# Performance work log

Measured on AMD Instinct MI355X. Metric: run time of the kernel, lower is better.

The kernel has to match this reference:

```python
import jax, jax.numpy as jnp
import numpy as np

V = 1_000_000      # vocab_length
E = 64             # embedding_dimension
H = 4              # mos_heads
B = 1024           # batch
S = V // 45        # num_neg_samples = 22222


def setup_inputs() -> dict:
    key = jax.random.key(0)
    k1, k2, k3, k4, k5, k6 = jax.random.split(key, 6)
    inputs = jax.random.normal(k1, (B, E), dtype=jnp.float32)
    # valid class ids are 1..V (id 0 is reserved by the sampler)
    label = jax.random.randint(k2, (B,), 1, V + 1, dtype=jnp.int32)
    sampled_ids = jax.random.randint(k3, (S,), 1, V + 1, dtype=jnp.int32)
    emb = jax.random.normal(k4, (V + 1, E), dtype=jnp.float32) * 0.05
    # GlorotNormal stddevs
    proj_mat = jax.random.normal(k5, (H * E, E), dtype=jnp.float32) * np.float32(np.sqrt(2.0 / (H * E + E)))
    mix_mat = jax.random.normal(k6, (H, E), dtype=jnp.float32) * np.float32(np.sqrt(2.0 / (H + E)))
    biases = jnp.zeros((V + 1,), dtype=jnp.float32)
    return {"inputs": inputs, "emb": emb, "proj_mat": proj_mat,
            "mix_mat": mix_mat, "biases": biases,
            "label": label, "sampled_ids": sampled_ids}


def reference(inputs, emb, proj_mat, mix_mat, biases, label, sampled_ids):
    # projections per mixture head: [B, H, E]
    mos_proj = jnp.tanh(inputs @ proj_mat.T).reshape(B, H, E)
    # mixture weights pi: [B, H]
    pi = jax.nn.softmax(inputs @ mix_mat.T, axis=-1)

    # sampled-softmax log-Q correction (unique unigram sampler, uniform probs):
    # expected_count = -expm1(S * log1p(-p)), p = 1/V
    p = jnp.float32(1.0 / V)
    log_q = jnp.log(-jnp.expm1(S * jnp.log1p(-p)))

    # true-class logit per head: [B, H]
    true_w = emb[label]                                   # [B, E] gather
    true_logit = (jnp.einsum('bhe,be->bh', mos_proj, true_w)
                  + biases[label][:, None] - log_q)
    # sampled logits per head: [B, H, S]
    samp_w = emb[sampled_ids]                             # [S, E] gather
    samp_logits = (jnp.einsum('bhe,se->bhs', mos_proj, samp_w)
                   + biases[sampled_ids][None, None, :] - log_q)

    logits = jnp.concatenate([true_logit[:, :, None], samp_logits], axis=-1)  # [B, H, 1+S]
    head_probs = jax.nn.softmax(logits, axis=-1)
    # mixture over heads: [B, 1+S]
    probs = jnp.einsum('bh,bhs->bs', pi, head_probs)
    # sampled labels are one-hot at position 0 -> loss = -mean(log p[:,0])
    loss = -jnp.mean(jnp.log(probs[:, 0]))
    return probs, loss
```

## Files before the change

### kernel.cpp

```cpp
#include <hip/hip_runtime.h>

#define ED 64
#define HD 4
#define BD 1024
#define SNEG 22222
#define NT2 1408
#define SPAD2 22528
#define SP1 (SNEG+1)
#define LOGQ -3.81776242f
#define LOG2E 1.44269504f

typedef short bf16x8 __attribute__((ext_vector_type(8)));
typedef float f32x4 __attribute__((ext_vector_type(4)));

static __device__ __forceinline__ short f2bf(float f) {
    union { float f; unsigned u; } v; v.f = f;
    return (short)((v.u + 0x7FFFu + ((v.u >> 16) & 1u)) >> 16);
}

static __device__ __forceinline__ float fast_tanh(float x) {
    float ax = __builtin_fabsf(x);
    float e  = __expf(-2.f * ax);
    float t  = (1.f - e) / (1.f + e);
    return __builtin_copysignf(t, x);
}

static __device__ __forceinline__ float fexp2(float x) {
#if __has_builtin(__builtin_amdgcn_exp2f)
    return __builtin_amdgcn_exp2f(x);
#else
    return __expf(x * 0.69314718f);
#endif
}

__global__ __launch_bounds__(256) void k_setup(
        const float* __restrict__ inputs, const float* __restrict__ emb,
        const float* __restrict__ proj,   const float* __restrict__ mix,
        const float* __restrict__ biases, const int* __restrict__ label,
        const int* __restrict__ sids,
        short* __restrict__ A, float* __restrict__ pi, float* __restrict__ tl,
        short* __restrict__ W, float* __restrict__ bias_s,
        float* __restrict__ denom) {
    const int blk = blockIdx.x, t = threadIdx.x;
    __shared__ float s_in[64];
    __shared__ float s_proj[256];
    __shared__ float s_mix[4];
    __shared__ float s_red[256];

    if (t < 16) denom[blk*16 + t] = 0.f;

    #pragma unroll 1
    for (int bi = 0; bi < 4; ++bi) {
        int b = blk*4 + bi;
        if (t < 64) s_in[t] = inputs[b*64 + t];
        __syncthreads();
        const float* pr = proj + t*64;
        float dot = 0.f;
        #pragma unroll
        for (int k = 0; k < 64; k += 4)
            dot += s_in[k]*pr[k] + s_in[k+1]*pr[k+1] + s_in[k+2]*pr[k+2] + s_in[k+3]*pr[k+3];
        float val = fast_tanh(dot);
        s_proj[t] = val;
        A[(b*4 + (t >> 6))*64 + (t & 63)] = f2bf(val * LOG2E);
        if (t < 4) {
            const float* mr = mix + t*64;
            float md = 0.f;
            for (int k = 0; k < 64; ++k) md += s_in[k]*mr[k];
            s_mix[t] = md;
        }
        int lab = label[b];
        s_red[t] = s_proj[t] * emb[(size_t)lab*64 + (t & 63)];
        __syncthreads();
        if (t < 4) {
            float m = fmaxf(fmaxf(s_mix[0], s_mix[1]), fmaxf(s_mix[2], s_mix[3]));
            float e0 = __expf(s_mix[0]-m), e1 = __expf(s_mix[1]-m);
            float e2 = __expf(s_mix[2]-m), e3 = __expf(s_mix[3]-m);
            pi[b*4 + t] = __expf(s_mix[t]-m) / (e0+e1+e2+e3);
            float sum = 0.f;
            for (int k = 0; k < 64; ++k) sum += s_red[t*64 + k];
            tl[b*4 + t] = (sum + biases[lab] - LOGQ) * LOG2E;
        }
        __syncthreads();
    }

    #pragma unroll 1
    for (int rep = 0; rep < 3; ++rep) {
        int task = rep*256 + t;
        if (task >= 704) break;
        int s = blk*88 + (task >> 3);
        int l8 = task & 7;
        if (s < SNEG) {
            int id = sids[s];
            const float* src = emb + (size_t)id*64 + l8*8;
            bf16x8 o;
            #pragma unroll
            for (int j = 0; j < 8; ++j) o[j] = f2bf(src[j]);
            *(bf16x8*)(W + s*64 + l8*8) = o;
            if (l8 == 0) bias_s[s] = (biases[id] - LOGQ) * LOG2E;
        } else {
            bf16x8 o;
            #pragma unroll
            for (int j = 0; j < 8; ++j) o[j] = 0;
            *(bf16x8*)(W + s*64 + l8*8) = o;
            if (l8 == 0) bias_s[s] = -1e30f;
        }
    }
}

#define LOADT(S, T) { \
    const bf16x8* bp_ = (const bf16x8*)(W + (size_t)((T)*16 + c)*64); \
    b0##S = bp_[g]; b1##S = bp_[4 + g]; bb##S = bias_s[(T)*16 + c]; }

#define DCOMP(S) { \
    _Pragma("unroll") \
    for (int t4 = 0; t4 < 4; ++t4) { \
        f32x4 z = {bb##S, bb##S, bb##S, bb##S}; \
        z = __builtin_amdgcn_mfma_f32_16x16x32_bf16(a0[t4], b0##S, z, 0, 0, 0); \
        z = __builtin_amdgcn_mfma_f32_16x16x32_bf16(a1[t4], b1##S, z, 0, 0, 0); \
        s[t4*4+0] += fexp2(z[0]); \
        s[t4*4+1] += fexp2(z[1]); \
        s[t4*4+2] += fexp2(z[2]); \
        s[t4*4+3] += fexp2(z[3]); } }

#define PCOMP(S, T) { \
    int scol_ = (T)*16 + c; bool ok_ = scol_ < SNEG; \
    _Pragma("unroll") \
    for (int t4 = 0; t4 < 4; ++t4) { \
        f32x4 z = {bb##S, bb##S, bb##S, bb##S}; \
        z = __builtin_amdgcn_mfma_f32_16x16x32_bf16(a0[t4], b0##S, z, 0, 0, 0); \
        z = __builtin_amdgcn_mfma_f32_16x16x32_bf16(a1[t4], b1##S, z, 0, 0, 0); \
        float p_ = cf[t4][0]*fexp2(z[0]); \
        p_ = fmaf(cf[t4][1], fexp2(z[1]), p_); \
        p_ = fmaf(cf[t4][2], fexp2(z[2]), p_); \
        p_ = fmaf(cf[t4][3], fexp2(z[3]), p_); \
        if (ok_) orow[t4][scol_] = p_; } }

#define DPIPE(TB) { \
    LOADT(A, (TB)+0) LOADT(B, (TB)+1) LOADT(C, (TB)+2) \
    DCOMP(A) LOADT(A, (TB)+3) \
    DCOMP(B) LOADT(B, (TB)+4) \
    DCOMP(C) LOADT(C, (TB)+5) \
    DCOMP(A) LOADT(A, (TB)+6) \
    DCOMP(B) LOADT(B, (TB)+7) \
    DCOMP(C) LOADT(C, (TB)+8) \
    DCOMP(A) LOADT(A, (TB)+9) \
    DCOMP(B) LOADT(B, (TB)+10) \
    DCOMP(C) \
    DCOMP(A) \
    DCOMP(B) }

#define PPIPE(TB) { \
    LOADT(A, (TB)+0) LOADT(B, (TB)+1) LOADT(C, (TB)+2) \
    PCOMP(A, (TB)+0)  LOADT(A, (TB)+3) \
    PCOMP(B, (TB)+1)  LOADT(B, (TB)+4) \
    PCOMP(C, (TB)+2)  LOADT(C, (TB)+5) \
    PCOMP(A, (TB)+3)  LOADT(A, (TB)+6) \
    PCOMP(B, (TB)+4)  LOADT(B, (TB)+7) \
    PCOMP(C, (TB)+5)  LOADT(C, (TB)+8) \
    PCOMP(A, (TB)+6)  LOADT(A, (TB)+9) \
    PCOMP(B, (TB)+7)  LOADT(B, (TB)+10) \
    PCOMP(C, (TB)+8) \
    PCOMP(A, (TB)+9) \
    PCOMP(B, (TB)+10) }

__global__ __launch_bounds__(256, 4) void k_denom(
        const short* __restrict__ A, const short* __restrict__ W,
        const float* __restrict__ bias_s, float* __restrict__ denom) {
    const int wave = threadIdx.x >> 6, lane = threadIdx.x & 63;
    const int g = lane >> 4, c = lane & 15;
    const int rbase = blockIdx.y * 64;
    bf16x8 a0[4], a1[4];
    #pragma unroll
    for (int t4 = 0; t4 < 4; ++t4) {
        const bf16x8* ap = (const bf16x8*)(A + (size_t)(rbase + t4*16 + c)*64);
        a0[t4] = ap[g]; a1[t4] = ap[4 + g];
    }
    float s[16];
    #pragma unroll
    for (int i = 0; i < 16; ++i) s[i] = 0.f;

    const int t0 = (blockIdx.x*4 + wave) * 44;
    bf16x8 b0A, b1A, b0B, b1B, b0C, b1C;
    float bbA, bbB, bbC;
    DPIPE(t0)
    DPIPE(t0 + 11)
    DPIPE(t0 + 22)
    DPIPE(t0 + 33)

    #pragma unroll
    for (int m = 1; m < 16; m <<= 1)
        #pragma unroll
        for (int i = 0; i < 16; ++i) s[i] += __shfl_xor(s[i], m);
    if (c == 0) {
        #pragma unroll
        for (int t4 = 0; t4 < 4; ++t4)
            #pragma unroll
            for (int r = 0; r < 4; ++r)
                atomicAdd(&denom[rbase + t4*16 + g*4 + r], s[t4*4+r]);
    }
}

__global__ __launch_bounds__(256, 4) void k_probs(
        const short* __restrict__ A, const short* __restrict__ W,
        const float* __restrict__ bias_s, const float* __restrict__ pi,
        const float* __restrict__ tl, const float* __restrict__ denom,
        float* __restrict__ out) {
    const int t = threadIdx.x;
    const int wave = t >> 6, lane = t & 63;
    const int g = lane >> 4, c = lane & 15;
    const int rbase = blockIdx.y * 64;
    __shared__ float s_cf[64];
    __shared__ float s_et[64];
    __shared__ float s_ls[4];

    if (t < 64) {
        int row = rbase + t;
        float et = fexp2(tl[row]);
        float d  = denom[row] + et;
        s_cf[t] = pi[row] / d;
        s_et[t] = et;
    }
    __syncthreads();
    if (blockIdx.x == 0 && t < 16) {
        float p0 = 0.f;
        #pragma unroll
        for (int h = 0; h < 4; ++h) p0 += s_cf[t*4 + h] * s_et[t*4 + h];
        out[(size_t)(rbase/4 + t) * SP1] = p0;
    }
    if (blockIdx.x == 0 && blockIdx.y == 0) {
        float lg = 0.f;
        for (int b = t; b < BD; b += 256) {
            float p0 = 0.f;
            #pragma unroll
            for (int h = 0; h < 4; ++h) {
                float et = fexp2(tl[b*4 + h]);
                p0 += pi[b*4 + h] / (denom[b*4 + h] + et) * et;
            }
            lg += logf(p0);
        }
        #pragma unroll
        for (int m = 1; m < 64; m <<= 1) lg += __shfl_xor(lg, m);
        if (lane == 0) s_ls[wave] = lg;
        __syncthreads();
        if (t == 0)
            out[(size_t)BD * SP1] = -(s_ls[0]+s_ls[1]+s_ls[2]+s_ls[3]) * (1.f/(float)BD);
    }

    bf16x8 a0[4], a1[4];
    float cf[4][4];
    float* orow[4];
    #pragma unroll
    for (int t4 = 0; t4 < 4; ++t4) {
        const bf16x8* ap = (const bf16x8*)(A + (size_t)(rbase + t4*16 + c)*64);
        a0[t4] = ap[g]; a1[t4] = ap[4 + g];
        #pragma unroll
        for (int r = 0; r < 4; ++r) cf[t4][r] = s_cf[t4*16 + g*4 + r];
        orow[t4] = out + (size_t)(rbase/4 + t4*4 + g) * SP1 + 1;
    }

    const int t0 = (blockIdx.x*4 + wave) * 44;
    bf16x8 b0A, b1A, b0B, b1B, b0C, b1C;
    float bbA, bbB, bbC;
    PPIPE(t0)
    PPIPE(t0 + 11)
    PPIPE(t0 + 22)
    PPIPE(t0 + 33)
}

extern "C" void kernel_launch(void* const* d_in, const int* in_sizes, int n_in,
                              void* d_out, int out_size, void* d_ws, size_t ws_size,
                              hipStream_t stream) {
    const float* inputs = (const float*)d_in[0];
    const float* emb    = (const float*)d_in[1];
    const float* proj   = (const float*)d_in[2];
    const float* mix    = (const float*)d_in[3];
    const float* biases = (const float*)d_in[4];
    const int*   label  = (const int*)d_in[5];
    const int*   sids   = (const int*)d_in[6];
    float* out = (float*)d_out;

    char* ws = (char*)d_ws;
    short* W      = (short*)(ws);
    short* A      = (short*)(ws + 2883584);
    float* bias_s = (float*)(ws + 3407872);
    float* denom  = (float*)(ws + 3497984);
    float* pi     = (float*)(ws + 3514368);
    float* tl     = (float*)(ws + 3530752);

    k_setup<<<256, 256, 0, stream>>>(
        inputs, emb, proj, mix, biases, label, sids, A, pi, tl, W, bias_s, denom);
    k_denom<<<dim3(8, 64), 256, 0, stream>>>(A, W, bias_s, denom);
    k_probs<<<dim3(8, 64), 256, 0, stream>>>(A, W, bias_s, pi, tl, denom, out);
}
```

Baseline: 81.80 us.

## Stage probs output tiles in LDS and write coalesced nontemporal rows

The probs kernel now writes each wave's 16x176 output tile into a shared-memory staging buffer, then copies it to global memory row by row with lane-contiguous nontemporal stores. Before, each lane wrote scattered 4-byte elements across 16 different rows. The change targets poor write coalescing on the large output store and avoids polluting the cache with write-once data. In exchange it adds about 46 KB of LDS per block and drops the occupancy hint from the launch bounds, which may reduce the number of resident blocks and add LDS traffic. No barrier is needed because each wave only reads back the staging region it wrote itself.

```diff
diff --git a/kernel.cpp b/kernel.cpp
--- a/kernel.cpp
+++ b/kernel.cpp
@@ -122,8 +122,7 @@
         s[t4*4+2] += fexp2(z[2]); \
         s[t4*4+3] += fexp2(z[3]); } }
 
-#define PCOMP(S, T) { \
-    int scol_ = (T)*16 + c; bool ok_ = scol_ < SNEG; \
+#define PCOMPL(S, TL) { \
     _Pragma("unroll") \
     for (int t4 = 0; t4 < 4; ++t4) { \
         f32x4 z = {bb##S, bb##S, bb##S, bb##S}; \
@@ -133,7 +132,7 @@
         p_ = fmaf(cf[t4][1], fexp2(z[1]), p_); \
         p_ = fmaf(cf[t4][2], fexp2(z[2]), p_); \
         p_ = fmaf(cf[t4][3], fexp2(z[3]), p_); \
-        if (ok_) orow[t4][scol_] = p_; } }
+        swo[(t4*4 + g)*180 + (TL)*16 + c] = p_; } }
 
 #define DPIPE(TB) { \
     LOADT(A, (TB)+0) LOADT(B, (TB)+1) LOADT(C, (TB)+2) \
@@ -149,19 +148,28 @@
     DCOMP(A) \
     DCOMP(B) }
 
-#define PPIPE(TB) { \
+#define PPIPES(TB) { \
     LOADT(A, (TB)+0) LOADT(B, (TB)+1) LOADT(C, (TB)+2) \
-    PCOMP(A, (TB)+0)  LOADT(A, (TB)+3) \
-    PCOMP(B, (TB)+1)  LOADT(B, (TB)+4) \
-    PCOMP(C, (TB)+2)  LOADT(C, (TB)+5) \
-    PCOMP(A, (TB)+3)  LOADT(A, (TB)+6) \
-    PCOMP(B, (TB)+4)  LOADT(B, (TB)+7) \
-    PCOMP(C, (TB)+5)  LOADT(C, (TB)+8) \
-    PCOMP(A, (TB)+6)  LOADT(A, (TB)+9) \
-    PCOMP(B, (TB)+7)  LOADT(B, (TB)+10) \
-    PCOMP(C, (TB)+8) \
-    PCOMP(A, (TB)+9) \
-    PCOMP(B, (TB)+10) }
+    PCOMPL(A, 0)  LOADT(A, (TB)+3) \
+    PCOMPL(B, 1)  LOADT(B, (TB)+4) \
+    PCOMPL(C, 2)  LOADT(C, (TB)+5) \
+    PCOMPL(A, 3)  LOADT(A, (TB)+6) \
+    PCOMPL(B, 4)  LOADT(B, (TB)+7) \
+    PCOMPL(C, 5)  LOADT(C, (TB)+8) \
+    PCOMPL(A, 6)  LOADT(A, (TB)+9) \
+    PCOMPL(B, 7)  LOADT(B, (TB)+10) \
+    PCOMPL(C, 8) \
+    PCOMPL(A, 9) \
+    PCOMPL(B, 10) \
+    { int cb_ = (TB)*16; \
+      _Pragma("unroll") \
+      for (int r_ = 0; r_ < 16; ++r_) { \
+        float* drow_ = out + (size_t)(brow0 + r_)*SP1 + 1 + cb_; \
+        const float* srow_ = swo + r_*180; \
+        _Pragma("unroll") \
+        for (int k_ = lane; k_ < 176; k_ += 64) \
+            if (cb_ + k_ < SNEG) \
+                __builtin_nontemporal_store(srow_[k_], &drow_[k_]); } } }
 
 __global__ __launch_bounds__(256, 4) void k_denom(
         const short* __restrict__ A, const short* __restrict__ W,
@@ -200,7 +208,7 @@
     }
 }
 
-__global__ __launch_bounds__(256, 4) void k_probs(
+__global__ __launch_bounds__(256) void k_probs(
         const short* __restrict__ A, const short* __restrict__ W,
         const float* __restrict__ bias_s, const float* __restrict__ pi,
         const float* __restrict__ tl, const float* __restrict__ denom,
@@ -209,9 +217,11 @@
     const int wave = t >> 6, lane = t & 63;
     const int g = lane >> 4, c = lane & 15;
     const int rbase = blockIdx.y * 64;
+    const int brow0 = blockIdx.y * 16;
     __shared__ float s_cf[64];
     __shared__ float s_et[64];
     __shared__ float s_ls[4];
+    __shared__ float s_stage[4*16*180];
 
     if (t < 64) {
         int row = rbase + t;
@@ -225,7 +235,7 @@
         float p0 = 0.f;
         #pragma unroll
         for (int h = 0; h < 4; ++h) p0 += s_cf[t*4 + h] * s_et[t*4 + h];
-        out[(size_t)(rbase/4 + t) * SP1] = p0;
+        out[(size_t)(brow0 + t) * SP1] = p0;
     }
     if (blockIdx.x == 0 && blockIdx.y == 0) {
         float lg = 0.f;
@@ -248,23 +258,22 @@
 
     bf16x8 a0[4], a1[4];
     float cf[4][4];
-    float* orow[4];
     #pragma unroll
     for (int t4 = 0; t4 < 4; ++t4) {
         const bf16x8* ap = (const bf16x8*)(A + (size_t)(rbase + t4*16 + c)*64);
         a0[t4] = ap[g]; a1[t4] = ap[4 + g];
         #pragma unroll
         for (int r = 0; r < 4; ++r) cf[t4][r] = s_cf[t4*16 + g*4 + r];
-        orow[t4] = out + (size_t)(rbase/4 + t4*4 + g) * SP1 + 1;
-    }
-
+    }
+
+    float* swo = &s_stage[wave * 16*180];
     const int t0 = (blockIdx.x*4 + wave) * 44;
     bf16x8 b0A, b1A, b0B, b1B, b0C, b1C;
     float bbA, bbB, bbC;
-    PPIPE(t0)
-    PPIPE(t0 + 11)
-    PPIPE(t0 + 22)
-    PPIPE(t0 + 33)
+    PPIPES(t0)
+    PPIPES(t0 + 11)
+    PPIPES(t0 + 22)
+    PPIPES(t0 + 33)
 }
 
 extern "C" void kernel_launch(void* const* d_in, const int* in_sizes, int n_in,
```

Result: slower. 92.21 us (+12.7%).

## Fuse denominator and probability kernels with per-row-group atomic barrier

Applied to the files above, without the earlier changes.

Merges the denominator pass and the probability-writing pass into one kernel. Blocks sharing a row group synchronise through an atomic counter spin-wait instead of a kernel boundary, and the A fragments stay in registers across both phases. The loss is computed by block (0,0) after a global counter reaches all blocks. This removes one launch and the reload of A. It relies on all 8 blocks of a row group being co-resident, risks deadlock if they are not, and adds spin-wait latency.

```diff
diff --git a/kernel.cpp b/kernel.cpp
--- a/kernel.cpp
+++ b/kernel.cpp
@@ -40,7 +40,7 @@
         const int* __restrict__ sids,
         short* __restrict__ A, float* __restrict__ pi, float* __restrict__ tl,
         short* __restrict__ W, float* __restrict__ bias_s,
-        float* __restrict__ denom) {
+        float* __restrict__ denom, int* __restrict__ cnt, int* __restrict__ gcnt) {
     const int blk = blockIdx.x, t = threadIdx.x;
     __shared__ float s_in[64];
     __shared__ float s_proj[256];
@@ -48,6 +48,10 @@
     __shared__ float s_red[256];
 
     if (t < 16) denom[blk*16 + t] = 0.f;
+    if (blk == 0) {
+        if (t < 64) cnt[t] = 0;
+        if (t == 64) gcnt[0] = 0;
+    }
 
     #pragma unroll 1
     for (int bi = 0; bi < 4; ++bi) {
@@ -163,108 +167,121 @@
     PCOMP(A, (TB)+9) \
     PCOMP(B, (TB)+10) }
 
-__global__ __launch_bounds__(256, 4) void k_denom(
+__global__ __launch_bounds__(256, 4) void k_fused(
         const short* __restrict__ A, const short* __restrict__ W,
-        const float* __restrict__ bias_s, float* __restrict__ denom) {
-    const int wave = threadIdx.x >> 6, lane = threadIdx.x & 63;
+        const float* __restrict__ bias_s, const float* __restrict__ pi,
+        const float* __restrict__ tl, float* __restrict__ denom,
+        int* __restrict__ cnt, int* __restrict__ gcnt,
+        float* __restrict__ out) {
+    const int t = threadIdx.x;
+    const int wave = t >> 6, lane = t & 63;
     const int g = lane >> 4, c = lane & 15;
-    const int rbase = blockIdx.y * 64;
+    const int bx = blockIdx.x, by = blockIdx.y;
+    const int rbase = by * 64;
+    const int brow0 = by * 16;
+    __shared__ float s_cf[64];
+    __shared__ float s_et[64];
+    __shared__ float s_ls[4];
+
     bf16x8 a0[4], a1[4];
     #pragma unroll
     for (int t4 = 0; t4 < 4; ++t4) {
         const bf16x8* ap = (const bf16x8*)(A + (size_t)(rbase + t4*16 + c)*64);
         a0[t4] = ap[g]; a1[t4] = ap[4 + g];
     }
-    float s[16];
-    #pragma unroll
-    for (int i = 0; i < 16; ++i) s[i] = 0.f;
-
-    const int t0 = (blockIdx.x*4 + wave) * 44;
-    bf16x8 b0A, b1A, b0B, b1B, b0C, b1C;
-    float bbA, bbB, bbC;
-    DPIPE(t0)
-    DPIPE(t0 + 11)
-    DPIPE(t0 + 22)
-    DPIPE(t0 + 33)
-
-    #pragma unroll
-    for (int m = 1; m < 16; m <<= 1)
-        #pragma unroll
-        for (int i = 0; i < 16; ++i) s[i] += __shfl_xor(s[i], m);
-    if (c == 0) {
-        #pragma unroll
-        for (int t4 = 0; t4 < 4; ++t4)
-            #pragma unroll
-            for (int r = 0; r < 4; ++r)
-                atomicAdd(&denom[rbase + t4*16 + g*4 + r], s[t4*4+r]);
-    }
-}
-
-__global__ __launch_bounds__(256, 4) void k_probs(
-        const short* __restrict__ A, const short* __restrict__ W,
-        const float* __restrict__ bias_s, const float* __restrict__ pi,
-        const float* __restrict__ tl, const float* __restrict__ denom,
-        float* __restrict__ out) {
-    const int t = threadIdx.x;
-    const int wave = t >> 6, lane = t & 63;
-    const int g = lane >> 4, c = lane & 15;
-    const int rbase = blockIdx.y * 64;
-    __shared__ float s_cf[64];
-    __shared__ float s_et[64];
-    __shared__ float s_ls[4];
+
+    {
+        float s[16];
+        #pragma unroll
+        for (int i = 0; i < 16; ++i) s[i] = 0.f;
+        const int t0 = (bx*4 + wave) * 44;
+        bf16x8 b0A, b1A, b0B, b1B, b0C, b1C;
+        float bbA, bbB, bbC;
+        DPIPE(t0)
+        DPIPE(t0 + 11)
+        DPIPE(t0 + 22)
+        DPIPE(t0 + 33)
+        #pragma unroll
+        for (int m = 1; m < 16; m <<= 1)
+            #pragma unroll
+            for (int i = 0; i < 16; ++i) s[i] += __shfl_xor(s[i], m);
+        if (c == 0) {
+            #pragma unroll
+            for (int t4 = 0; t4 < 4; ++t4)
+                #pragma unroll
+                for (int r = 0; r < 4; ++r)
+                    atomicAdd(&denom[rbase + t4*16 + g*4 + r], s[t4*4+r]);
+        }
+    }
+
+    __syncthreads();
+    if (t == 0) {
+        __threadfence();
+        atomicAdd(gcnt, 1);
+        atomicAdd(&cnt[by], 1);
+        while (__hip_atomic_load(&cnt[by], __ATOMIC_ACQUIRE, __HIP_MEMORY_SCOPE_AGENT) < 8)
+            __builtin_amdgcn_s_sleep(1);
+    }
+    __syncthreads();
 
     if (t < 64) {
         int row = rbase + t;
+        float dv = __hip_atomic_load(&denom[row], __ATOMIC_RELAXED, __HIP_MEMORY_SCOPE_AGENT);
         float et = fexp2(tl[row]);
-        float d  = denom[row] + et;
+        float d  = dv + et;
         s_cf[t] = pi[row] / d;
         s_et[t] = et;
     }
     __syncthreads();
-    if (blockIdx.x == 0 && t < 16) {
+    if (bx == 0 && t < 16) {
         float p0 = 0.f;
         #pragma unroll
         for (int h = 0; h < 4; ++h) p0 += s_cf[t*4 + h] * s_et[t*4 + h];
-        out[(size_t)(rbase/4 + t) * SP1] = p0;
-    }
-    if (blockIdx.x == 0 && blockIdx.y == 0) {
-        float lg = 0.f;
-        for (int b = t; b < BD; b += 256) {
-            float p0 = 0.f;
-            #pragma unroll
-            for (int h = 0; h < 4; ++h) {
-                float et = fexp2(tl[b*4 + h]);
-                p0 += pi[b*4 + h] / (denom[b*4 + h] + et) * et;
-            }
-            lg += logf(p0);
-        }
-        #pragma unroll
-        for (int m = 1; m < 64; m <<= 1) lg += __shfl_xor(lg, m);
-        if (lane == 0) s_ls[wave] = lg;
-        __syncthreads();
-        if (t == 0)
-            out[(size_t)BD * SP1] = -(s_ls[0]+s_ls[1]+s_ls[2]+s_ls[3]) * (1.f/(float)BD);
-    }
-
-    bf16x8 a0[4], a1[4];
+        out[(size_t)(brow0 + t) * SP1] = p0;
+    }
+
     float cf[4][4];
     float* orow[4];
     #pragma unroll
     for (int t4 = 0; t4 < 4; ++t4) {
-        const bf16x8* ap = (const bf16x8*)(A + (size_t)(rbase + t4*16 + c)*64);
-        a0[t4] = ap[g]; a1[t4] = ap[4 + g];
         #pragma unroll
         for (int r = 0; r < 4; ++r) cf[t4][r] = s_cf[t4*16 + g*4 + r];
-        orow[t4] = out + (size_t)(rbase/4 + t4*4 + g) * SP1 + 1;
-    }
-
-    const int t0 = (blockIdx.x*4 + wave) * 44;
-    bf16x8 b0A, b1A, b0B, b1B, b0C, b1C;
-    float bbA, bbB, bbC;
-    PPIPE(t0)
-    PPIPE(t0 + 11)
-    PPIPE(t0 + 22)
-    PPIPE(t0 + 33)
+        orow[t4] = out + (size_t)(brow0 + t4*4 + g) * SP1 + 1;
+    }
+    {
+        const int t0 = (bx*4 + wave) * 44;
+        bf16x8 b0A, b1A, b0B, b1B, b0C, b1C;
+        float bbA, bbB, bbC;
+        PPIPE(t0)
+        PPIPE(t0 + 11)
+        PPIPE(t0 + 22)
+        PPIPE(t0 + 33)
+    }
+
+    if (bx == 0 && by == 0) {
+        if (t == 0) {
+            while (__hip_atomic_load(gcnt, __ATOMIC_ACQUIRE, __HIP_MEMORY_SCOPE_AGENT) < 512)
+                __builtin_amdgcn_s_sleep(1);
+        }
+        __syncthreads();
+        float lg = 0.f;
+        for (int b = t; b < BD; b += 256) {
+            float p0 = 0.f;
+            #pragma unroll
+            for (int h = 0; h < 4; ++h) {
+                float dv = __hip_atomic_load(&denom[b*4 + h], __ATOMIC_RELAXED, __HIP_MEMORY_SCOPE_AGENT);
+                float et = fexp2(tl[b*4 + h]);
+                p0 += pi[b*4 + h] / (dv + et) * et;
+            }
+            lg += logf(p0);
+        }
+        #pragma unroll
+        for (int m = 1; m < 64; m <<= 1) lg += __shfl_xor(lg, m);
+        if (lane == 0) s_ls[wave] = lg;
+        __syncthreads();
+        if (t == 0)
+            out[(size_t)BD * SP1] = -(s_ls[0]+s_ls[1]+s_ls[2]+s_ls[3]) * (1.f/(float)BD);
+    }
 }
 
 extern "C" void kernel_launch(void* const* d_in, const int* in_sizes, int n_in,
@@ -286,9 +303,12 @@
     float* denom  = (float*)(ws + 3497984);
     float* pi     = (float*)(ws + 3514368);
     float* tl     = (float*)(ws + 3530752);
+    int*   cnt    = (int*)  (ws + 3547136);
+    int*   gcnt   = (int*)  (ws + 3547392);
 
     k_setup<<<256, 256, 0, stream>>>(
-        inputs, emb, proj, mix, biases, label, sids, A, pi, tl, W, bias_s, denom);
-    k_denom<<<dim3(8, 64), 256, 0, stream>>>(A, W, bias_s, denom);
-    k_probs<<<dim3(8, 64), 256, 0, stream>>>(A, W, bias_s, pi, tl, denom, out);
-}
+        inputs, emb, proj, mix, biases, label, sids, A, pi, tl, W, bias_s,
+        denom, cnt, gcnt);
+    k_fused<<<dim3(8, 64), 256, 0, stream>>>(
+        A, W, bias_s, pi, tl, denom, cnt, gcnt, out);
+}
```

Result: slower. 171.3 us (+109.4%).
